# Kernel optimization log

Hardware: AMD Instinct MI355X
Metric: run time of the kernel (lower is better)

## Reference

```python
import jax, jax.numpy as jnp
import numpy as np

B, T, D, H = 4, 2048, 1024, 16
HD = D // H          # head_size = 64
FF = 16 * D          # FeedForward hidden = 16*n_embd per source
EPS = 1e-5


def layer_norm(x, g, b):
    mu = jnp.mean(x, axis=-1, keepdims=True)
    var = jnp.mean(jnp.square(x - mu), axis=-1, keepdims=True)
    return (x - mu) * jax.lax.rsqrt(var + EPS) * g + b


def setup_inputs() -> dict:
    key = jax.random.key(0)
    ks = jax.random.split(key, 17)
    s_d = 1.0 / np.sqrt(D)
    s_ff = 1.0 / np.sqrt(FF)
    return {
        "x": jax.random.normal(ks[0], (B, T, D), jnp.float32),
        # per-head Q/K/V linears, batched over heads: [H, D, HD]
        "Wq": jax.random.normal(ks[1], (H, D, HD), jnp.float32) * s_d,
        "bq": jax.random.normal(ks[2], (H, HD), jnp.float32) * s_d,
        "Wk": jax.random.normal(ks[3], (H, D, HD), jnp.float32) * s_d,
        "bk": jax.random.normal(ks[4], (H, HD), jnp.float32) * s_d,
        "Wv": jax.random.normal(ks[5], (H, D, HD), jnp.float32) * s_d,
        "bv": jax.random.normal(ks[6], (H, HD), jnp.float32) * s_d,
        "Wo": jax.random.normal(ks[7], (D, D), jnp.float32) * s_d,
        "bo": jax.random.normal(ks[8], (D,), jnp.float32) * s_d,
        "ln1_g": jnp.ones((D,), jnp.float32),
        "ln1_b": jnp.zeros((D,), jnp.float32),
        "W1": jax.random.normal(ks[9], (D, FF), jnp.float32) * s_d,
        "b1": jax.random.normal(ks[10], (FF,), jnp.float32) * s_d,
        "W2": jax.random.normal(ks[11], (FF, D), jnp.float32) * s_ff,
        "b2": jax.random.normal(ks[12], (D,), jnp.float32) * s_ff,
        "ln2_g": jnp.ones((D,), jnp.float32),
        "ln2_b": jnp.zeros((D,), jnp.float32),
    }


def reference(x, Wq, bq, Wk, bk, Wv, bv, Wo, bo, ln1_g, ln1_b,
              W1, b1, W2, b2, ln2_g, ln2_b):
    # --- multi-head causal self-attention (all heads batched) ---
    q = jnp.einsum('btd,hdk->bhtk', x, Wq) + bq[None, :, None, :]
    k = jnp.einsum('btd,hdk->bhtk', x, Wk) + bk[None, :, None, :]
    v = jnp.einsum('btd,hdk->bhtk', x, Wv) + bv[None, :, None, :]
    scores = jnp.einsum('bhtk,bhsk->bhts', q, k) / np.sqrt(HD)
    causal = jnp.tril(jnp.ones((T, T), bool))
    scores = jnp.where(causal, scores, -jnp.inf)
    attn = jax.nn.softmax(scores, axis=-1)
    out = jnp.einsum('bhts,bhsk->bhtk', attn, v)
    out = out.transpose(0, 2, 1, 3).reshape(x.shape[0], x.shape[1], H * HD)
    attn_out = out @ Wo + bo
    # --- post-LN residual structure, as in the source ---
    out1 = layer_norm(x + attn_out, ln1_g, ln1_b)
    ff = jax.nn.relu(out1 @ W1 + b1) @ W2 + b2
    out2 = layer_norm(out1 + ff, ln2_g, ln2_b)
    return out2
```

## Files before the change

### kernel.cpp

```cpp
#include <hip/hip_runtime.h>

typedef unsigned short u16;
typedef unsigned int   u32;
typedef __attribute__((ext_vector_type(8))) short short8;
typedef __attribute__((ext_vector_type(4))) float f32x4;

#define DEV static __device__ __forceinline__

DEV u16 f2bf(float x) {
  union { float f; u32 u; } c; c.f = x;
  u32 r = c.u + 0x7fffu + ((c.u >> 16) & 1u);
  return (u16)(r >> 16);
}

struct __align__(8) us4 { u16 a, b, c, d; };

DEV void gload16(const void* g, void* l) {
  __builtin_amdgcn_global_load_lds(
      (const __attribute__((address_space(1))) void*)g,
      (__attribute__((address_space(3))) void*)l, 16, 0, 0);
}

template<int EPI>
__global__ __launch_bounds__(256)
void gemm_bt(const u16* __restrict__ A, const u16* __restrict__ Bt,
             const float* __restrict__ bias, const float* __restrict__ resid,
             float* __restrict__ outf, u16* __restrict__ outb,
             u16* __restrict__ q_out, u16* __restrict__ k_out, u16* __restrict__ vt_out,
             int M, int N, int K)
{
  __shared__ __align__(16) u16 As[128 * 64];
  __shared__ __align__(16) u16 Bs[128 * 64];
  const int tid = threadIdx.x;
  const int lane = tid & 63;
  const int wave = tid >> 6;
  const int wm = wave >> 1, wn = wave & 1;
  const int lo = lane & 15, hi = lane >> 4;

  const int nwg = gridDim.x * gridDim.y;
  int bid = blockIdx.y * gridDim.x + blockIdx.x;
  bid = (bid & 7) * (nwg >> 3) + (bid >> 3);
  const int bm = (bid / gridDim.x) * 128;
  const int bn = (bid % gridDim.x) * 128;

  const int kchunk = K / gridDim.z;
  const int kbeg = blockIdx.z * kchunk;
  const int kend = kbeg + kchunk;

  f32x4 zero = {0.f, 0.f, 0.f, 0.f};
  f32x4 acc[4][4];
#pragma unroll
  for (int i = 0; i < 4; ++i)
#pragma unroll
    for (int j = 0; j < 4; ++j) acc[i][j] = zero;

  for (int k0 = kbeg; k0 < kend; k0 += 64) {
#pragma unroll
    for (int i = 0; i < 4; ++i) {
      int slot = i * 4096 + tid * 16;
      int row  = slot >> 7;
      int c16  = (slot >> 4) & 7;
      int gc   = (c16 ^ (row & 7)) * 8;
      gload16(A  + (size_t)(bm + row) * K + k0 + gc,
              (char*)As + i * 4096 + wave * 1024);
      gload16(Bt + (size_t)(bn + row) * K + k0 + gc,
              (char*)Bs + i * 4096 + wave * 1024);
    }
    __syncthreads();
#pragma unroll
    for (int kk = 0; kk < 2; ++kk) {
      short8 a[4], b[4];
      int ks = kk * 4 + hi;
#pragma unroll
      for (int mi = 0; mi < 4; ++mi) {
        int row = wm * 64 + mi * 16 + lo;
        a[mi] = *(const short8*)&As[row * 64 + ((ks ^ (row & 7)) * 8)];
      }
#pragma unroll
      for (int ni = 0; ni < 4; ++ni) {
        int row = wn * 64 + ni * 16 + lo;
        b[ni] = *(const short8*)&Bs[row * 64 + ((ks ^ (row & 7)) * 8)];
      }
#pragma unroll
      for (int mi = 0; mi < 4; ++mi)
#pragma unroll
        for (int ni = 0; ni < 4; ++ni)
          acc[mi][ni] = __builtin_amdgcn_mfma_f32_16x16x32_bf16(
              a[mi], b[ni], acc[mi][ni], 0, 0, 0);
    }
    __syncthreads();
  }

#pragma unroll
  for (int mi = 0; mi < 4; ++mi) {
#pragma unroll
    for (int ni = 0; ni < 4; ++ni) {
      int col = bn + wn * 64 + ni * 16 + lo;
#pragma unroll
      for (int r = 0; r < 4; ++r) {
        int row = bm + wm * 64 + mi * 16 + hi * 4 + r;
        float v = acc[mi][ni][r];
        if (EPI == 0) {
          v += bias[col];
          int qkv = col >> 10, wc = col & 1023, h = wc >> 6, hd = wc & 63;
          int b_ = row >> 11, t = row & 2047;
          u16 bv = f2bf(v);
          if (qkv == 0)
            q_out[((size_t)((b_ * 16 + h) * 2048 + t)) * 64 + hd] = bv;
          else if (qkv == 1)
            k_out[((size_t)((b_ * 16 + h) * 2048 + t)) * 64 + hd] = bv;
          else
            vt_out[((size_t)((b_ * 16 + h) * 64 + hd)) * 2048 + t] = bv;
        } else if (EPI == 1) {
          v += bias[col] + resid[(size_t)row * N + col];
          outf[(size_t)row * N + col] = v;
        } else if (EPI == 2) {
          v += bias[col];
          v = v > 0.f ? v : 0.f;
          outb[(size_t)row * N + col] = f2bf(v);
        } else {
          atomicAdd(&outf[(size_t)row * N + col], v);
        }
      }
    }
  }
}

__global__ __launch_bounds__(256)
void attn_kernel(const u16* __restrict__ Q, const u16* __restrict__ Kb,
                 const u16* __restrict__ Vt, u16* __restrict__ O)
{
  __shared__ __align__(16) u16 Ks[2][64 * 64];
  __shared__ __align__(16) u16 Vs[2][64 * 64];
  __shared__ __align__(16) u16 Pl[4][16 * 80];
  const int tid = threadIdx.x, lane = tid & 63, w = tid >> 6;
  const int lo = lane & 15, hi = lane >> 4;
  const int bh = blockIdx.y;
  const int qt = gridDim.x - 1 - blockIdx.x;
  const int q0 = qt * 64;

  const size_t qbase = ((size_t)bh * 2048 + q0 + w * 16 + lo) * 64;
  short8 qf[2];
  qf[0] = *(const short8*)(Q + qbase + hi * 8);
  qf[1] = *(const short8*)(Q + qbase + 32 + hi * 8);

  const int slot0 = tid * 16;
  const int srow0 = slot0 >> 7;
  const int sgc0  = (((slot0 >> 4) & 7) ^ (srow0 & 7)) * 8;
  const int slot1 = 4096 + tid * 16;
  const int srow1 = slot1 >> 7;
  const int sgc1  = (((slot1 >> 4) & 7) ^ (srow1 & 7)) * 8;
  const u16* kRow0 = Kb + ((size_t)bh * 2048 + srow0) * 64 + sgc0;
  const u16* kRow1 = Kb + ((size_t)bh * 2048 + srow1) * 64 + sgc1;
  const u16* vRow0 = Vt + ((size_t)bh * 64 + srow0) * 2048 + sgc0;
  const u16* vRow1 = Vt + ((size_t)bh * 64 + srow1) * 2048 + sgc1;
  const int ldsOff = tid * 16 - (tid * 16 & 4095) ? 0 : 0;

#define ATTN_STAGE(buf, s)                                                   \
  do {                                                                       \
    gload16(kRow0 + (size_t)(s) * 64 * 64,                                   \
            (char*)Ks + (buf) * 8192 + ((tid * 16) & 4095) +                 \
            ((tid * 16) >> 12) * 0);                                         \
    gload16(kRow1 + (size_t)(s) * 64 * 64,                                   \
            (char*)Ks + (buf) * 8192 + 4096 + ((tid * 16) & 4095));          \
    gload16(vRow0 + (size_t)(s) * 64,                                        \
            (char*)Vs + (buf) * 8192 + ((tid * 16) & 4095));                 \
    gload16(vRow1 + (size_t)(s) * 64,                                        \
            (char*)Vs + (buf) * 8192 + 4096 + ((tid * 16) & 4095));          \
  } while (0)

  float m[4]    = {-1e30f, -1e30f, -1e30f, -1e30f};
  float lsum[4] = {0.f, 0.f, 0.f, 0.f};
  f32x4 zero = {0.f, 0.f, 0.f, 0.f};
  f32x4 oacc[4];
#pragma unroll
  for (int i = 0; i < 4; ++i) oacc[i] = zero;

  const int smax = qt;
  ATTN_STAGE(0, 0);
  int cur = 0;

  for (int s = 0; s <= smax; ++s) {
    if (s < smax) {
      ATTN_STAGE(cur ^ 1, s + 1);
      asm volatile("s_waitcnt vmcnt(4)" ::: "memory");
    } else {
      asm volatile("s_waitcnt vmcnt(0)" ::: "memory");
    }
    __builtin_amdgcn_s_barrier();

    const u16* ksb = Ks[cur];
    const u16* vsb = Vs[cur];

    f32x4 sacc[4];
#pragma unroll
    for (int i = 0; i < 4; ++i) sacc[i] = zero;
#pragma unroll
    for (int ni = 0; ni < 4; ++ni)
#pragma unroll
      for (int kk = 0; kk < 2; ++kk) {
        int row = ni * 16 + lo;
        short8 kf = *(const short8*)&ksb[row * 64 + (((kk * 4 + hi) ^ (row & 7)) * 8)];
        sacc[ni] = __builtin_amdgcn_mfma_f32_16x16x32_bf16(qf[kk], kf, sacc[ni], 0, 0, 0);
      }

    const bool diag = (s == smax);
    float pvv[4][4];
#pragma unroll
    for (int r = 0; r < 4; ++r) {
      int qrow = q0 + w * 16 + hi * 4 + r;
      float mx = -1e30f;
#pragma unroll
      for (int ni = 0; ni < 4; ++ni) {
        float v = sacc[ni][r] * 0.125f;
        int kv = s * 64 + ni * 16 + lo;
        if (diag && kv > qrow) v = -1e30f;
        pvv[ni][r] = v;
        mx = fmaxf(mx, v);
      }
#pragma unroll
      for (int msk = 1; msk < 16; msk <<= 1) mx = fmaxf(mx, __shfl_xor(mx, msk));
      float mnew = fmaxf(m[r], mx);
      float corr = __expf(m[r] - mnew);
      m[r] = mnew;
      float rs = 0.f;
#pragma unroll
      for (int ni = 0; ni < 4; ++ni) {
        float p = __expf(pvv[ni][r] - mnew);
        pvv[ni][r] = p;
        rs += p;
      }
#pragma unroll
      for (int msk = 1; msk < 16; msk <<= 1) rs += __shfl_xor(rs, msk);
      lsum[r] = lsum[r] * corr + rs;
#pragma unroll
      for (int nd = 0; nd < 4; ++nd) oacc[nd][r] *= corr;
    }

#pragma unroll
    for (int ni = 0; ni < 4; ++ni) {
      int chunk = ni * 2 + (lo >> 3);
      int wi    = lo & 7;
#pragma unroll
      for (int r = 0; r < 4; ++r) {
        int rowp = hi * 4 + r;
        Pl[w][rowp * 80 + (((chunk ^ (rowp & 7)) << 3) | wi)] = f2bf(pvv[ni][r]);
      }
    }

#pragma unroll
    for (int kk = 0; kk < 2; ++kk) {
      short8 pa = *(const short8*)&Pl[w][lo * 80 + (((kk * 4 + hi) ^ (lo & 7)) << 3)];
#pragma unroll
      for (int nd = 0; nd < 4; ++nd) {
        int row = nd * 16 + lo;
        short8 vf = *(const short8*)&vsb[row * 64 + (((kk * 4 + hi) ^ (row & 7)) * 8)];
        oacc[nd] = __builtin_amdgcn_mfma_f32_16x16x32_bf16(pa, vf, oacc[nd], 0, 0, 0);
      }
    }
    __builtin_amdgcn_s_barrier();
    cur ^= 1;
  }
#undef ATTN_STAGE

  const int b_ = bh >> 4, h_ = bh & 15;
#pragma unroll
  for (int r = 0; r < 4; ++r) {
    int t = q0 + w * 16 + hi * 4 + r;
    float inv = 1.f / lsum[r];
    size_t base = ((size_t)b_ * 2048 + t) * 1024 + h_ * 64;
#pragma unroll
    for (int nd = 0; nd < 4; ++nd)
      O[base + nd * 16 + lo] = f2bf(oacc[nd][r] * inv);
  }
  (void)ldsOff;
}

__global__ __launch_bounds__(256)
void ln_kernel(const float* __restrict__ in, const float* __restrict__ g,
               const float* __restrict__ bp, float* __restrict__ outf,
               u16* __restrict__ outb,
               float* __restrict__ seed_out, const float* __restrict__ seed_bias)
{
  const int row = blockIdx.x, t = threadIdx.x;
  const f32x4 v = *(const f32x4*)(in + (size_t)row * 1024 + t * 4);
  float s  = v[0] + v[1] + v[2] + v[3];
  float sq = v[0] * v[0] + v[1] * v[1] + v[2] * v[2] + v[3] * v[3];
#pragma unroll
  for (int off = 32; off; off >>= 1) {
    s  += __shfl_down(s, off);
    sq += __shfl_down(sq, off);
  }
  __shared__ float red[8];
  const int lane = t & 63, w = t >> 6;
  if (lane == 0) { red[w] = s; red[4 + w] = sq; }
  __syncthreads();
  s  = red[0] + red[1] + red[2] + red[3];
  sq = red[4] + red[5] + red[6] + red[7];
  float mu  = s * (1.f / 1024.f);
  float var = sq * (1.f / 1024.f) - mu * mu;
  float rstd = rsqrtf(var + 1e-5f);
  const f32x4 gv = *(const f32x4*)(g + t * 4);
  const f32x4 bv = *(const f32x4*)(bp + t * 4);
  f32x4 o;
#pragma unroll
  for (int j = 0; j < 4; ++j) o[j] = (v[j] - mu) * rstd * gv[j] + bv[j];
  *(f32x4*)(outf + (size_t)row * 1024 + t * 4) = o;
  if (outb) {
    us4 ob = {f2bf(o[0]), f2bf(o[1]), f2bf(o[2]), f2bf(o[3])};
    *(us4*)(outb + (size_t)row * 1024 + t * 4) = ob;
  }
  if (seed_out) {
    const f32x4 sb = *(const f32x4*)(seed_bias + t * 4);
    f32x4 so = {o[0] + sb[0], o[1] + sb[1], o[2] + sb[2], o[3] + sb[3]};
    *(f32x4*)(seed_out + (size_t)row * 1024 + t * 4) = so;
  }
}

__global__ __launch_bounds__(256)
void cvt_bf16(const float* __restrict__ src, u16* __restrict__ dst, int n4)
{
  int i = blockIdx.x * 256 + threadIdx.x;
  if (i < n4) {
    f32x4 v = *(const f32x4*)(src + (size_t)i * 4);
    us4 o = {f2bf(v[0]), f2bf(v[1]), f2bf(v[2]), f2bf(v[3])};
    *(us4*)(dst + (size_t)i * 4) = o;
  }
}

__global__ __launch_bounds__(256)
void transpose_cvt(const float* __restrict__ src, u16* __restrict__ dst, int R, int C)
{
  __shared__ float tile[64][65];
  const int c0 = blockIdx.x * 64, r0 = blockIdx.y * 64;
  const int t = threadIdx.x;
  const int rl = t >> 4, c4 = (t & 15) * 4;
#pragma unroll
  for (int i = 0; i < 4; ++i) {
    f32x4 v = *(const f32x4*)(src + (size_t)(r0 + rl + i * 16) * C + c0 + c4);
    tile[rl + i * 16][c4 + 0] = v[0];
    tile[rl + i * 16][c4 + 1] = v[1];
    tile[rl + i * 16][c4 + 2] = v[2];
    tile[rl + i * 16][c4 + 3] = v[3];
  }
  __syncthreads();
#pragma unroll
  for (int j = 0; j < 16; ++j) {
    int o = t + j * 256;
    int c = o >> 6, r = o & 63;
    dst[(size_t)(c0 + c) * R + r0 + r] = f2bf(tile[r][c]);
  }
}

__global__ __launch_bounds__(256)
void qkv_pack(const float* __restrict__ Wq, const float* __restrict__ Wk,
              const float* __restrict__ Wv, u16* __restrict__ Wt)
{
  const float* src = blockIdx.z == 0 ? Wq : (blockIdx.z == 1 ? Wk : Wv);
  src += (size_t)blockIdx.y * 1024 * 64;
  __shared__ float tile[64][65];
  const int k0 = blockIdx.x * 64;
  const int t = threadIdx.x;
  const int rl = t >> 4, c4 = (t & 15) * 4;
#pragma unroll
  for (int i = 0; i < 4; ++i) {
    f32x4 v = *(const f32x4*)(src + (size_t)(k0 + rl + i * 16) * 64 + c4);
    tile[rl + i * 16][c4 + 0] = v[0];
    tile[rl + i * 16][c4 + 1] = v[1];
    tile[rl + i * 16][c4 + 2] = v[2];
    tile[rl + i * 16][c4 + 3] = v[3];
  }
  __syncthreads();
  size_t nbase = (size_t)blockIdx.z * 1024 + blockIdx.y * 64;
#pragma unroll
  for (int j = 0; j < 16; ++j) {
    int o = t + j * 256;
    int hd = o >> 6, r = o & 63;
    Wt[(nbase + hd) * 1024 + k0 + r] = f2bf(tile[r][hd]);
  }
}

__global__ void bias_pack(const float* __restrict__ bq, const float* __restrict__ bk,
                          const float* __restrict__ bv, float* __restrict__ out)
{
  int i = blockIdx.x * 256 + threadIdx.x;
  if (i < 3072) {
    const float* s = (i >> 10) == 0 ? bq : ((i >> 10) == 1 ? bk : bv);
    out[i] = s[i & 1023];
  }
}

extern "C" void kernel_launch(void* const* d_in, const int* in_sizes, int n_in,
                              void* d_out, int out_size, void* d_ws, size_t ws_size,
                              hipStream_t stream)
{
  const float* x    = (const float*)d_in[0];
  const float* Wq   = (const float*)d_in[1];
  const float* bq   = (const float*)d_in[2];
  const float* Wk   = (const float*)d_in[3];
  const float* bk   = (const float*)d_in[4];
  const float* Wv   = (const float*)d_in[5];
  const float* bv   = (const float*)d_in[6];
  const float* Wo   = (const float*)d_in[7];
  const float* bo   = (const float*)d_in[8];
  const float* ln1g = (const float*)d_in[9];
  const float* ln1b = (const float*)d_in[10];
  const float* W1   = (const float*)d_in[11];
  const float* b1   = (const float*)d_in[12];
  const float* W2   = (const float*)d_in[13];
  const float* b2   = (const float*)d_in[14];
  const float* ln2g = (const float*)d_in[15];
  const float* ln2b = (const float*)d_in[16];
  float* out = (float*)d_out;

  char* ws = (char*)d_ws;
  const size_t MB = 1ull << 20;
  u16*   Wqkvt = (u16*)(ws + 0);
  float* bqkv  = (float*)(ws + 6 * MB);
  u16*   Wot   = (u16*)(ws + 7 * MB);
  u16*   W1t   = (u16*)(ws + 9 * MB);
  u16*   W2t   = (u16*)(ws + 41 * MB);
  u16*   out1b = (u16*)(ws + 73 * MB);
  float* y1    = (float*)(ws + 89 * MB);
  u16*   Xb    = (u16*)(ws + 121 * MB);
  u16*   Qb    = (u16*)(ws + 137 * MB);
  u16*   Kb    = (u16*)(ws + 153 * MB);
  u16*   Vt    = (u16*)(ws + 169 * MB);
  u16*   attnb = (u16*)(ws + 185 * MB);
  u16*   h_buf = (u16*)(ws + 121 * MB);
  float* y2    = out;

  const int nchunks = (ws_size >= 377 * MB) ? 1 : 4;
  const int Mc      = 8192 / nchunks;
  const int zsplit  = (nchunks == 1) ? 4 : 8;

  cvt_bf16<<<8192, 256, 0, stream>>>(x, Xb, 8192 * 1024 / 4);
  qkv_pack<<<dim3(16, 16, 3), 256, 0, stream>>>(Wq, Wk, Wv, Wqkvt);
  bias_pack<<<12, 256, 0, stream>>>(bq, bk, bv, bqkv);
  transpose_cvt<<<dim3(16, 16), 256, 0, stream>>>(Wo, Wot, 1024, 1024);
  transpose_cvt<<<dim3(256, 16), 256, 0, stream>>>(W1, W1t, 1024, 16384);
  transpose_cvt<<<dim3(16, 256), 256, 0, stream>>>(W2, W2t, 16384, 1024);

  gemm_bt<0><<<dim3(24, 64), 256, 0, stream>>>(Xb, Wqkvt, bqkv, nullptr,
      nullptr, nullptr, Qb, Kb, Vt, 8192, 3072, 1024);

  attn_kernel<<<dim3(32, 64), 256, 0, stream>>>(Qb, Kb, Vt, attnb);

  gemm_bt<1><<<dim3(8, 64), 256, 0, stream>>>(attnb, Wot, bo, x,
      y1, nullptr, nullptr, nullptr, nullptr, 8192, 1024, 1024);

  ln_kernel<<<8192, 256, 0, stream>>>(y1, ln1g, ln1b, y1, out1b, y2, b2);

  for (int c = 0; c < nchunks; ++c) {
    gemm_bt<2><<<dim3(128, Mc / 128), 256, 0, stream>>>(
        out1b + (size_t)c * Mc * 1024, W1t, b1, nullptr,
        nullptr, h_buf, nullptr, nullptr, nullptr, Mc, 16384, 1024);
    gemm_bt<3><<<dim3(8, Mc / 128, zsplit), 256, 0, stream>>>(
        h_buf, W2t, nullptr, nullptr,
        y2 + (size_t)c * Mc * 1024, nullptr, nullptr, nullptr, nullptr,
        Mc, 1024, 16384);
  }

  ln_kernel<<<8192, 256, 0, stream>>>(y2, ln2g, ln2b, out, nullptr,
                                      nullptr, nullptr);

  (void)in_sizes; (void)n_in; (void)out_size;
}
```

Before: 1.485 ms.

## Use exp2 softmax with lazy rescaling, MFMA priority hints, and two-chunk FFN path

The attention softmax now folds log2(e) into the score scale and uses exp2f. It skips the running-max correction unless some row's max grows by more than a threshold, which removes most per-tile rescale multiplies and exps. s_setprio raises wave priority around the MFMA sections so matrix work is issued ahead of other waves. A new intermediate workspace tier lets the FFN run in two chunks instead of four when memory allows. The lazy rescale lets unnormalized values grow up to about 2^11, a small numerical risk.

```diff
diff --git a/kernel.cpp b/kernel.cpp
--- a/kernel.cpp
+++ b/kernel.cpp
@@ -138,6 +138,7 @@
   const int bh = blockIdx.y;
   const int qt = gridDim.x - 1 - blockIdx.x;
   const int q0 = qt * 64;
+  const float SC2 = 0.18033688011112042f;
 
   const size_t qbase = ((size_t)bh * 2048 + q0 + w * 16 + lo) * 64;
   short8 qf[2];
@@ -154,13 +155,11 @@
   const u16* kRow1 = Kb + ((size_t)bh * 2048 + srow1) * 64 + sgc1;
   const u16* vRow0 = Vt + ((size_t)bh * 64 + srow0) * 2048 + sgc0;
   const u16* vRow1 = Vt + ((size_t)bh * 64 + srow1) * 2048 + sgc1;
-  const int ldsOff = tid * 16 - (tid * 16 & 4095) ? 0 : 0;
 
 #define ATTN_STAGE(buf, s)                                                   \
   do {                                                                       \
     gload16(kRow0 + (size_t)(s) * 64 * 64,                                   \
-            (char*)Ks + (buf) * 8192 + ((tid * 16) & 4095) +                 \
-            ((tid * 16) >> 12) * 0);                                         \
+            (char*)Ks + (buf) * 8192 + ((tid * 16) & 4095));                 \
     gload16(kRow1 + (size_t)(s) * 64 * 64,                                   \
             (char*)Ks + (buf) * 8192 + 4096 + ((tid * 16) & 4095));          \
     gload16(vRow0 + (size_t)(s) * 64,                                        \
@@ -195,6 +194,7 @@
     f32x4 sacc[4];
 #pragma unroll
     for (int i = 0; i < 4; ++i) sacc[i] = zero;
+    __builtin_amdgcn_s_setprio(1);
 #pragma unroll
     for (int ni = 0; ni < 4; ++ni)
 #pragma unroll
@@ -203,16 +203,17 @@
         short8 kf = *(const short8*)&ksb[row * 64 + (((kk * 4 + hi) ^ (row & 7)) * 8)];
         sacc[ni] = __builtin_amdgcn_mfma_f32_16x16x32_bf16(qf[kk], kf, sacc[ni], 0, 0, 0);
       }
+    __builtin_amdgcn_s_setprio(0);
 
     const bool diag = (s == smax);
-    float pvv[4][4];
+    float pvv[4][4], mxr[4];
 #pragma unroll
     for (int r = 0; r < 4; ++r) {
       int qrow = q0 + w * 16 + hi * 4 + r;
       float mx = -1e30f;
 #pragma unroll
       for (int ni = 0; ni < 4; ++ni) {
-        float v = sacc[ni][r] * 0.125f;
+        float v = sacc[ni][r] * SC2;
         int kv = s * 64 + ni * 16 + lo;
         if (diag && kv > qrow) v = -1e30f;
         pvv[ni][r] = v;
@@ -220,21 +221,35 @@
       }
 #pragma unroll
       for (int msk = 1; msk < 16; msk <<= 1) mx = fmaxf(mx, __shfl_xor(mx, msk));
-      float mnew = fmaxf(m[r], mx);
-      float corr = __expf(m[r] - mnew);
-      m[r] = mnew;
+      mxr[r] = mx;
+    }
+
+    bool need = (mxr[0] > m[0] + 11.f) || (mxr[1] > m[1] + 11.f) ||
+                (mxr[2] > m[2] + 11.f) || (mxr[3] > m[3] + 11.f);
+    if (__any(need)) {
+#pragma unroll
+      for (int r = 0; r < 4; ++r) {
+        float mnew = fmaxf(m[r], mxr[r]);
+        float corr = exp2f(m[r] - mnew);
+        m[r] = mnew;
+        lsum[r] *= corr;
+#pragma unroll
+        for (int nd = 0; nd < 4; ++nd) oacc[nd][r] *= corr;
+      }
+    }
+
+#pragma unroll
+    for (int r = 0; r < 4; ++r) {
       float rs = 0.f;
 #pragma unroll
       for (int ni = 0; ni < 4; ++ni) {
-        float p = __expf(pvv[ni][r] - mnew);
+        float p = exp2f(pvv[ni][r] - m[r]);
         pvv[ni][r] = p;
         rs += p;
       }
 #pragma unroll
       for (int msk = 1; msk < 16; msk <<= 1) rs += __shfl_xor(rs, msk);
-      lsum[r] = lsum[r] * corr + rs;
-#pragma unroll
-      for (int nd = 0; nd < 4; ++nd) oacc[nd][r] *= corr;
+      lsum[r] += rs;
     }
 
 #pragma unroll
@@ -248,6 +263,7 @@
       }
     }
 
+    __builtin_amdgcn_s_setprio(1);
 #pragma unroll
     for (int kk = 0; kk < 2; ++kk) {
       short8 pa = *(const short8*)&Pl[w][lo * 80 + (((kk * 4 + hi) ^ (lo & 7)) << 3)];
@@ -258,6 +274,7 @@
         oacc[nd] = __builtin_amdgcn_mfma_f32_16x16x32_bf16(pa, vf, oacc[nd], 0, 0, 0);
       }
     }
+    __builtin_amdgcn_s_setprio(0);
     __builtin_amdgcn_s_barrier();
     cur ^= 1;
   }
@@ -273,7 +290,6 @@
     for (int nd = 0; nd < 4; ++nd)
       O[base + nd * 16 + lo] = f2bf(oacc[nd][r] * inv);
   }
-  (void)ldsOff;
 }
 
 __global__ __launch_bounds__(256)
@@ -430,7 +446,7 @@
   u16*   h_buf = (u16*)(ws + 121 * MB);
   float* y2    = out;
 
-  const int nchunks = (ws_size >= 377 * MB) ? 1 : 4;
+  const int nchunks = (ws_size >= 377 * MB) ? 1 : (ws_size >= 249 * MB) ? 2 : 4;
   const int Mc      = 8192 / nchunks;
   const int zsplit  = (nchunks == 1) ? 4 : 8;
 
```

Result: slower. 1.544 ms (+3.9%).
